# Optimization experiments

Hardware: AMD Instinct MI355X
Metric: run time of the kernel (lower is better)

## Reference

```python
import jax, jax.numpy as jnp
import numpy as np

M, B, S, D, H = 3, 32, 256, 768, 1024
LN_EPS = 1e-5


def _ln(x, g, b):
    m = jnp.mean(x, axis=-1, keepdims=True)
    v = jnp.mean((x - m) ** 2, axis=-1, keepdims=True)
    return (x - m) / jnp.sqrt(v + LN_EPS) * g + b


def setup_inputs() -> dict:
    key = jax.random.key(0)
    ks = jax.random.split(key, 16)
    sc = 0.02  # weight init scale
    return {
        "feats": jax.random.normal(ks[0], (M, B, S, D), jnp.float32),
        "Wq": jax.random.normal(ks[1], (M, D, D), jnp.float32) * sc,
        "bq": jnp.zeros((M, D), jnp.float32),
        "Wk": jax.random.normal(ks[2], (M, D, D), jnp.float32) * sc,
        "bk": jnp.zeros((M, D), jnp.float32),
        "Wv": jax.random.normal(ks[3], (M, D, D), jnp.float32) * sc,
        "bv": jnp.zeros((M, D), jnp.float32),
        "pgq_w": jax.random.normal(ks[4], (M, D), jnp.float32) * sc,
        "pgq_b": jnp.zeros((M,), jnp.float32),
        "pgk_w": jax.random.normal(ks[5], (M, D), jnp.float32) * sc,
        "pgk_b": jnp.zeros((M,), jnp.float32),
        "mu_w": jax.random.normal(ks[6], (M, D), jnp.float32) * sc,
        "mu_b": jnp.zeros((M,), jnp.float32),
        "lv_w": jax.random.normal(ks[7], (M, D), jnp.float32) * sc,
        "lv_b": jnp.zeros((M,), jnp.float32),
        "dyn": jnp.ones((1,), jnp.float32),
        "WE_w": jax.random.normal(ks[8], (M, D, D), jnp.float32) * sc,
        "WE_b": jnp.zeros((M, D), jnp.float32),
        "Wh_w": jax.random.normal(ks[9], (M, D, D), jnp.float32) * sc,
        "Wh_b": jnp.zeros((M, D), jnp.float32),
        "Wqc_w": jax.random.normal(ks[10], (M, D, D), jnp.float32) * sc,
        "Wqc_b": jnp.zeros((M, D), jnp.float32),
        "lnE_g": jnp.ones((M, D), jnp.float32),
        "lnE_b": jnp.zeros((M, D), jnp.float32),
        "lnG_g": jnp.ones((M, D), jnp.float32),
        "lnG_b": jnp.zeros((M, D), jnp.float32),
        "out_w": jax.random.normal(ks[11], (D * M, H), jnp.float32) * sc,
        "out_b": jnp.zeros((H,), jnp.float32),
        "eps": jax.random.normal(ks[12], (M, M - 1, B, S, 1), jnp.float32),
    }


def reference(feats, Wq, bq, Wk, bk, Wv, bv, pgq_w, pgq_b, pgk_w, pgk_b,
              mu_w, mu_b, lv_w, lv_b, dyn, WE_w, WE_b, Wh_w, Wh_b, Wqc_w, Wqc_b,
              lnE_g, lnE_b, lnG_g, lnG_b, out_w, out_b, eps):
    # batched per-modality projections: [M,B,S,D]
    Qs = jnp.einsum('mbsd,mde->mbse', feats, Wq) + bq[:, None, None, :]
    Ks = jnp.einsum('mbsd,mde->mbse', feats, Wk) + bk[:, None, None, :]
    Vs = jnp.einsum('mbsd,mde->mbse', feats, Wv) + bv[:, None, None, :]
    scale = 1.0 / jnp.sqrt(jnp.float32(D))

    kl = jnp.float32(0.0)
    outs = []
    for i in range(M):
        Qi = Qs[i]  # [B,S,D]
        mu = jnp.einsum('bsd,d->bs', Qi, mu_w[i])[..., None] + mu_b[i]      # [B,S,1]
        lv = jnp.einsum('bsd,d->bs', Qi, lv_w[i])[..., None] + lv_b[i]      # [B,S,1]
        std = jnp.exp(0.5 * lv)
        pq_base = jax.nn.sigmoid(
            jnp.einsum('bsd,d->bs', Qi, pgq_w[i])[..., None] + pgq_b[i])    # [B,S,1]
        kl_i = -0.5 * jnp.sum(1.0 + lv - mu ** 2 - jnp.exp(lv))
        agg = jnp.zeros_like(Qi)
        cnt = 0
        for j in range(M):
            if j == i:
                continue
            d_gate = mu + dyn * std * eps[i, cnt]  # reparameterization
            cnt += 1
            kl = kl + kl_i
            g = jax.nn.sigmoid(d_gate)             # [B,S,1]
            p_q = pq_base * g
            p_k = jax.nn.sigmoid(
                jnp.einsum('bsd,d->bs', Ks[j], pgk_w[i])[..., None] + pgk_b[i]) * g
            A = jnp.einsum('bqd,bkd->bqk', Qi, Ks[j]) * scale
            A = A * p_q * jnp.swapaxes(p_k, 1, 2)  # pregated scores
            W = jax.nn.softmax(A, axis=-1)
            agg = agg + jnp.einsum('bqk,bkd->bqd', W, Vs[j])
        # CAG
        E = jax.nn.relu(agg @ WE_w[i] + WE_b[i])
        G = jax.nn.relu(agg @ Wh_w[i] + Wh_b[i] + Qi @ Wqc_w[i] + Wqc_b[i])
        Ci = _ln(E, lnE_g[i], lnE_b[i]) * _ln(G, lnG_g[i], lnG_b[i])
        outs.append(Ci)
    fused = jnp.concatenate(outs, axis=-1)[:, 0, :]  # [B, M*D]
    out = fused @ out_w + out_b                       # [B, H]
    return out, kl
```

## Files before the change

### kernel.cpp

```cpp
#include <hip/hip_runtime.h>

#define M 3
#define B 32
#define S 256
#define D 768
#define H 1024
#define MD (M * D)
#define NP (M * (M - 1))
#define SCALE 0.03608439182435161f
#define LN_EPS 1e-5f

#define OFF_WMU   0
#define OFF_WLV   2304
#define OFF_WPGQ  4608
#define OFF_WPK   6912
#define OFF_CMU   11520
#define OFF_CLV   11523
#define OFF_CPGQ  11526
#define OFF_CPK   11529
#define OFF_MU    11552
#define OFF_LV    36128
#define OFF_PKPRE 60704
#define OFF_PQPRE 109856
#define OFF_Q     109952
#define OFF_QBK   183680
#define OFF_QK    183872
#define OFF_MLH   331328
#define OFF_AGG   332864
#define OFF_E     406592
#define OFF_G     480320
#define OFF_FUSED 554048
#define OFF_KL    627776
#define OFF_FSUM  627840
#define OFF_WKT   1217664
#define OFF_ARENA 2987136
#define OFF_ARENA2 6526080
#define OFF_KLP   11834496

__device__ __forceinline__ float wave_reduce(float v) {
    #pragma unroll
    for (int o = 32; o > 0; o >>= 1) v += __shfl_down(v, o, 64);
    return v;
}

__device__ __forceinline__ float sigmoidf(float x) {
    return 1.0f / (1.0f + __expf(-x));
}

__device__ __forceinline__ float dot4(float4 a, float4 b) {
    return a.x * b.x + a.y * b.y + a.z * b.z + a.w * b.w;
}

__device__ __forceinline__ void fma4(float4& a, float s, float4 w) {
    a.x += s * w.x; a.y += s * w.y; a.z += s * w.z; a.w += s * w.w;
}

__global__ __launch_bounds__(256) void k_prep2(const float* feats,
        const float* Wq, const float* Wk,
        const float* bq, const float* bk,
        const float* mu_w, const float* mu_b, const float* lv_w, const float* lv_b,
        const float* pgq_w, const float* pgq_b, const float* pgk_w, const float* pgk_b,
        float* ws) {
    int blk = blockIdx.x;
    if (blk < 72) {
        int mat = blk / 12, rg = blk % 12;
        const float* Wm; const float *va, *vb, *vc;
        float *oa, *ob, *oc; int nv;
        if (mat < 3) {
            int i = mat;
            Wm = Wq + i * D * D;
            va = mu_w + i * D; vb = lv_w + i * D; vc = pgq_w + i * D;
            oa = ws + OFF_WMU + i * D; ob = ws + OFF_WLV + i * D; oc = ws + OFF_WPGQ + i * D;
            nv = 3;
        } else {
            int j = mat - 3;
            int i1 = (j == 0) ? 1 : 0, i2 = (j == 2) ? 1 : 2;
            int p1 = 2 * i1 + ((j < i1) ? j : j - 1);
            int p2 = 2 * i2 + ((j < i2) ? j : j - 1);
            Wm = Wk + j * D * D;
            va = pgk_w + i1 * D; vb = pgk_w + i2 * D; vc = va;
            oa = ws + OFF_WPK + p1 * D; ob = ws + OFF_WPK + p2 * D; oc = oa;
            nv = 2;
        }
        int wave = threadIdx.x >> 6, lane = threadIdx.x & 63;
        const float4* va4 = (const float4*)va;
        const float4* vb4 = (const float4*)vb;
        const float4* vc4 = (const float4*)vc;
        float4 A0 = va4[lane], A1 = va4[lane + 64], A2 = va4[lane + 128];
        float4 B0 = vb4[lane], B1 = vb4[lane + 64], B2 = vb4[lane + 128];
        float4 C0 = vc4[lane], C1 = vc4[lane + 64], C2 = vc4[lane + 128];
        int base = rg * 64 + wave * 16;
        for (int r = 0; r < 16; r += 2) {
            const float4* rowP = (const float4*)(Wm + (base + r) * D);
            const float4* rowQ = (const float4*)(Wm + (base + r + 1) * D);
            float4 x0 = rowP[lane], x1 = rowP[lane + 64], x2 = rowP[lane + 128];
            float4 y0 = rowQ[lane], y1 = rowQ[lane + 64], y2 = rowQ[lane + 128];
            float daP = dot4(x0, A0) + dot4(x1, A1) + dot4(x2, A2);
            float dbP = dot4(x0, B0) + dot4(x1, B1) + dot4(x2, B2);
            float dcP = dot4(x0, C0) + dot4(x1, C1) + dot4(x2, C2);
            float daQ = dot4(y0, A0) + dot4(y1, A1) + dot4(y2, A2);
            float dbQ = dot4(y0, B0) + dot4(y1, B1) + dot4(y2, B2);
            float dcQ = dot4(y0, C0) + dot4(y1, C1) + dot4(y2, C2);
            daP = wave_reduce(daP); dbP = wave_reduce(dbP);
            daQ = wave_reduce(daQ); dbQ = wave_reduce(dbQ);
            if (nv == 3) { dcP = wave_reduce(dcP); dcQ = wave_reduce(dcQ); }
            if (lane == 0) {
                oa[base + r] = daP; ob[base + r] = dbP;
                oa[base + r + 1] = daQ; ob[base + r + 1] = dbQ;
                if (nv == 3) { oc[base + r] = dcP; oc[base + r + 1] = dcQ; }
            }
        }
    } else if (blk < 87) {
        int job = blk - 72;
        const float *a, *bvec; float bias; float* out;
        if (job < 3)      { int i = job;     a = bq + i * D; bvec = mu_w + i * D;  bias = mu_b[i];  out = ws + OFF_CMU + i; }
        else if (job < 6) { int i = job - 3; a = bq + i * D; bvec = lv_w + i * D;  bias = lv_b[i];  out = ws + OFF_CLV + i; }
        else if (job < 9) { int i = job - 6; a = bq + i * D; bvec = pgq_w + i * D; bias = pgq_b[i]; out = ws + OFF_CPGQ + i; }
        else {
            int p = job - 9, i = p / 2, c = p % 2, j = c + (c >= i ? 1 : 0);
            a = bk + j * D; bvec = pgk_w + i * D; bias = pgk_b[i]; out = ws + OFF_CPK + p;
        }
        int t = threadIdx.x;
        float part = 0.f;
        if (t < 192) part = dot4(((const float4*)a)[t], ((const float4*)bvec)[t]);
        part = wave_reduce(part);
        __shared__ float r[4];
        if ((t & 63) == 0) r[t >> 6] = part;
        __syncthreads();
        if (t == 0) *out = r[0] + r[1] + r[2] + r[3] + bias;
    } else if (blk < 519) {
        int r = blk - 87;
        int j = r / 144; r = r % 144;
        int d0 = (r / 12) * 64, e0 = (r % 12) * 64;
        __shared__ float tile[64][65];
        const float* src = Wk + j * D * D;
        for (int idx = threadIdx.x; idx < 4096; idx += 256) {
            int rr = idx / 64, cc = idx % 64;
            tile[rr][cc] = src[(d0 + rr) * D + e0 + cc];
        }
        __syncthreads();
        float* dst = ws + OFF_WKT + j * D * D;
        for (int idx = threadIdx.x; idx < 4096; idx += 256) {
            int rr = idx / 64, cc = idx % 64;
            dst[(e0 + rr) * D + d0 + cc] = tile[cc][rr];
        }
    } else {
        int qb = blk - 519;
        int i = qb / 96, r = qb % 96, bg = r / 24, kc = r % 24;
        int kbase = kc * 32;
        __shared__ __align__(16) float xs[32][8];
        for (int idx = threadIdx.x; idx < 256; idx += 256) {
            int d = idx & 31, bb = idx >> 5;
            xs[d][bb] = feats[((size_t)(i * B + bg * 8 + bb) * S) * D + kbase + d];
        }
        __syncthreads();
        if (threadIdx.x < 192) {
            int e4 = threadIdx.x * 4;
            const float* Wm = Wq + i * D * D + kbase * D + e4;
            float4 acc[8];
            #pragma unroll
            for (int bb = 0; bb < 8; bb++) acc[bb] = make_float4(0.f, 0.f, 0.f, 0.f);
            for (int k = 0; k < 32; k++) {
                float4 w = *(const float4*)(Wm + k * D);
                float4 x0 = *(const float4*)&xs[k][0];
                float4 x1 = *(const float4*)&xs[k][4];
                fma4(acc[0], x0.x, w); fma4(acc[1], x0.y, w);
                fma4(acc[2], x0.z, w); fma4(acc[3], x0.w, w);
                fma4(acc[4], x1.x, w); fma4(acc[5], x1.y, w);
                fma4(acc[6], x1.z, w); fma4(acc[7], x1.w, w);
            }
            #pragma unroll
            for (int bb = 0; bb < 8; bb++)
                *(float4*)&ws[OFF_ARENA + kc * 73728 + (i * 32 + bg * 8 + bb) * 768 + e4] = acc[bb];
        }
    }
}

__global__ __launch_bounds__(256) void k_redQ(const float* bq, const float* bk, float* ws) {
    int blk = blockIdx.x;
    int i = blk / B, b = blk % B;
    int fbase = (i * B + b) * D;
    int t = threadIdx.x;
    __shared__ float4 qsh[192];
    __shared__ float redsh[8];
    if (t < 192) {
        float4 a = *(const float4*)&bq[i * D + t * 4];
        #pragma unroll
        for (int kc = 0; kc < 24; kc++) {
            float4 v = *(const float4*)&ws[OFF_ARENA + kc * 73728 + fbase + t * 4];
            a.x += v.x; a.y += v.y; a.z += v.z; a.w += v.w;
        }
        *(float4*)&ws[OFF_Q + fbase + t * 4] = a;
        qsh[t] = a;
    }
    __syncthreads();
    int jA = (i == 0) ? 1 : 0, jB = (i == 2) ? 1 : 2;
    float pA_ = 0.f, pB_ = 0.f;
    if (t < 192) {
        float4 q = qsh[t];
        pA_ = dot4(q, *(const float4*)&bk[jA * D + t * 4]);
        pB_ = dot4(q, *(const float4*)&bk[jB * D + t * 4]);
    }
    pA_ = wave_reduce(pA_); pB_ = wave_reduce(pB_);
    int wave = t >> 6, lane = t & 63;
    if (lane == 0) { redsh[wave] = pA_; redsh[4 + wave] = pB_; }
    __syncthreads();
    if (t == 0) {
        ws[OFF_QBK + (2 * i) * B + b]     = redsh[0] + redsh[1] + redsh[2] + redsh[3];
        ws[OFF_QBK + (2 * i + 1) * B + b] = redsh[4] + redsh[5] + redsh[6] + redsh[7];
    }
}

__global__ __launch_bounds__(256) void k_stats2(const float* feats,
        const float* bq, const float* bk, float* ws) {
    int blk = blockIdx.x;
    if (blk < 576) {
        int j = blk / 192, r = blk % 192, vg = r / 24, kc = r % 24;
        int kbase = kc * 32;
        int i1 = (j == 0) ? 1 : 0, i2 = (j == 2) ? 1 : 2;
        __shared__ __align__(16) float xs[32][8];
        for (int idx = threadIdx.x; idx < 256; idx += 256) {
            int d = idx & 31, v = idx >> 5;
            int v64 = vg * 8 + v;
            int i_ = (v64 < 32) ? i1 : i2, b = v64 & 31;
            xs[d][v] = ws[OFF_Q + (i_ * 32 + b) * 768 + kbase + d];
        }
        __syncthreads();
        if (threadIdx.x < 192) {
            int e4 = threadIdx.x * 4;
            const float* Wm = ws + OFF_WKT + j * D * D + kbase * D + e4;
            float4 acc[8];
            #pragma unroll
            for (int bb = 0; bb < 8; bb++) acc[bb] = make_float4(0.f, 0.f, 0.f, 0.f);
            for (int k = 0; k < 32; k++) {
                float4 w = *(const float4*)(Wm + k * D);
                float4 x0 = *(const float4*)&xs[k][0];
                float4 x1 = *(const float4*)&xs[k][4];
                fma4(acc[0], x0.x, w); fma4(acc[1], x0.y, w);
                fma4(acc[2], x0.z, w); fma4(acc[3], x0.w, w);
                fma4(acc[4], x1.x, w); fma4(acc[5], x1.y, w);
                fma4(acc[6], x1.z, w); fma4(acc[7], x1.w, w);
            }
            #pragma unroll
            for (int v = 0; v < 8; v++)
                *(float4*)&ws[OFF_ARENA2 + kc * 147456 + (j * 64 + vg * 8 + v) * 768 + e4] = acc[v];
        }
    } else {
        int blk2 = blk - 576;
        __shared__ float klred[4];
        int wave = threadIdx.x >> 6, lane = threadIdx.x & 63;
        int m = blk2 / 512;
        int row0 = blk2 * 16 + wave * 4;
        int i1 = (m == 0) ? 1 : 0, i2 = (m == 2) ? 1 : 2;
        int p0 = 2 * i1 + ((m < i1) ? m : m - 1);
        int p1 = 2 * i2 + ((m < i2) ? m : m - 1);
        const float4* wmu  = (const float4*)(ws + OFF_WMU + m * D);
        const float4* wlv  = (const float4*)(ws + OFF_WLV + m * D);
        const float4* wpgq = (const float4*)(ws + OFF_WPGQ + m * D);
        const float4* wpk0 = (const float4*)(ws + OFF_WPK + p0 * D);
        const float4* wpk1 = (const float4*)(ws + OFF_WPK + p1 * D);
        float4 U0 = wmu[lane],  U1 = wmu[lane + 64],  U2 = wmu[lane + 128];
        float4 L0 = wlv[lane],  L1 = wlv[lane + 64],  L2 = wlv[lane + 128];
        float4 Q0 = wpgq[lane], Q1 = wpgq[lane + 64], Q2 = wpgq[lane + 128];
        float4 P0 = wpk0[lane], P1 = wpk0[lane + 64], P2 = wpk0[lane + 128];
        float4 R0 = wpk1[lane], R1 = wpk1[lane + 64], R2 = wpk1[lane + 128];
        float4 x[4][3];
        #pragma unroll
        for (int rr = 0; rr < 4; rr++) {
            const float4* f = (const float4*)(feats + (size_t)(row0 + rr) * D);
            x[rr][0] = f[lane]; x[rr][1] = f[lane + 64]; x[rr][2] = f[lane + 128];
        }
        float amu[4], alv[4], apgq[4], apk0[4], apk1[4];
        #pragma unroll
        for (int rr = 0; rr < 4; rr++) {
            amu[rr]  = dot4(x[rr][0], U0) + dot4(x[rr][1], U1) + dot4(x[rr][2], U2);
            alv[rr]  = dot4(x[rr][0], L0) + dot4(x[rr][1], L1) + dot4(x[rr][2], L2);
            apgq[rr] = dot4(x[rr][0], Q0) + dot4(x[rr][1], Q1) + dot4(x[rr][2], Q2);
            apk0[rr] = dot4(x[rr][0], P0) + dot4(x[rr][1], P1) + dot4(x[rr][2], P2);
            apk1[rr] = dot4(x[rr][0], R0) + dot4(x[rr][1], R1) + dot4(x[rr][2], R2);
        }
        #pragma unroll
        for (int rr = 0; rr < 4; rr++) {
            amu[rr] = wave_reduce(amu[rr]);  alv[rr] = wave_reduce(alv[rr]);
            apgq[rr] = wave_reduce(apgq[rr]);
            apk0[rr] = wave_reduce(apk0[rr]); apk1[rr] = wave_reduce(apk1[rr]);
        }
        if (lane == 0) {
            float cmu = ws[OFF_CMU + m], clv = ws[OFF_CLV + m];
            float cpgq = ws[OFF_CPGQ + m];
            float cpk0 = ws[OFF_CPK + p0], cpk1 = ws[OFF_CPK + p1];
            float klsum = 0.f;
            #pragma unroll
            for (int rr = 0; rr < 4; rr++) {
                int row = row0 + rr;
                int rem = row % (B * S);
                int b = rem / S, s = rem % S;
                float muv = amu[rr] + cmu;
                float lvv = alv[rr] + clv;
                ws[OFF_MU + row] = muv;
                ws[OFF_LV + row] = lvv;
                ws[OFF_PKPRE + (p0 * B + b) * S + s] = apk0[rr] + cpk0;
                ws[OFF_PKPRE + (p1 * B + b) * S + s] = apk1[rr] + cpk1;
                if (s == 0) ws[OFF_PQPRE + m * B + b] = apgq[rr] + cpgq;
                klsum += 1.0f + lvv - muv * muv - __expf(lvv);
            }
            klred[wave] = klsum;
        }
        __syncthreads();
        if (threadIdx.x == 0)
            ws[OFF_KLP + blk2] = klred[0] + klred[1] + klred[2] + klred[3];
    }
}

__global__ __launch_bounds__(256) void k_redqk(float* ws) {
    int idx = blockIdx.x * 256 + threadIdx.x;
    int fidx = idx * 4;
    int row = fidx / 768, d = fidx % 768;
    int j = row / 64, v64 = row % 64;
    int b = v64 & 31, islot = v64 >> 5;
    int i_ = islot ? ((j == 2) ? 1 : 2) : ((j == 0) ? 1 : 0);
    int p = 2 * i_ + ((j < i_) ? j : j - 1);
    float4 a = make_float4(0.f, 0.f, 0.f, 0.f);
    #pragma unroll
    for (int kc = 0; kc < 24; kc++) {
        float4 v = *(const float4*)&ws[OFF_ARENA2 + kc * 147456 + fidx];
        a.x += v.x; a.y += v.y; a.z += v.z; a.w += v.w;
    }
    *(float4*)&ws[OFF_QK + (p * B + b) * D + d] = a;
}

__global__ __launch_bounds__(1024) void k_attn(const float* feats, const float* eps,
                                               const float* dyn, float* ws) {
    int blk = blockIdx.x;
    int j = blk / 128, r = blk % 128, b = r >> 2, h = r & 3;
    int i1 = (j == 0) ? 1 : 0, i2 = (j == 2) ? 1 : 2;
    int pA = 2 * i1 + ((j < i1) ? j : j - 1);
    int pB = 2 * i2 + ((j < i2) ? j : j - 1);
    __shared__ __align__(16) float q[2][768];
    __shared__ float pk[2][64];
    __shared__ float sch[2][32], wch[2][32];
    __shared__ float scal[2], pqs[2];
    int t = threadIdx.x;
    float dynv = dyn[0];
    if (t < 384) {
        int slot = t / 192;
        int d4 = (t % 192) * 4;
        int p = slot ? pB : pA;
        *(float4*)&q[slot][d4] = *(const float4*)&ws[OFF_QK + (p * B + b) * D + d4];
    } else if (t < 512) {
        int t2 = t - 384, slot = t2 >> 6, tt = t2 & 63;
        int k = h * 64 + tt;
        int iq = slot ? i2 : i1, p = slot ? pB : pA;
        float mu = ws[OFF_MU + (iq * B + b) * S + k];
        float lv = ws[OFF_LV + (iq * B + b) * S + k];
        float e  = eps[(p * B + b) * S + k];
        float g  = sigmoidf(mu + dynv * __expf(0.5f * lv) * e);
        pk[slot][tt] = sigmoidf(ws[OFF_PKPRE + (p * B + b) * S + k]) * g;
    } else if (t < 514) {
        int slot = t - 512;
        int iq = slot ? i2 : i1, p = slot ? pB : pA;
        float mu0 = ws[OFF_MU + (iq * B + b) * S];
        float lv0 = ws[OFF_LV + (iq * B + b) * S];
        float e0  = eps[(p * B + b) * S];
        float g0  = sigmoidf(mu0 + dynv * __expf(0.5f * lv0) * e0);
        pqs[slot] = sigmoidf(ws[OFF_PQPRE + iq * B + b]) * g0;
    }
    __syncthreads();
    float qbkA = ws[OFF_QBK + pA * B + b];
    float qbkB = ws[OFF_QBK + pB * B + b];
    const float* fb = feats + (size_t)((j * B + b) * S + h * 64) * D;
    float accA = 0.f, accB = 0.f;
    float mloc = -1e30f, lloc = 0.f;
    int w = t >> 6, lane = t & 63;
    for (int c = 0; c < 2; c++) {
        #pragma unroll
        for (int e = 0; e < 2; e++) {
            int rloc = c * 32 + (w << 1) + e;
            const float4* f4 = (const float4*)(fb + (size_t)rloc * D);
            float4 x0 = f4[lane], x1 = f4[lane + 64], x2 = f4[lane + 128];
            const float4* qa4 = (const float4*)&q[0][0];
            const float4* qb4 = (const float4*)&q[1][0];
            float dA = dot4(x0, qa4[lane]) + dot4(x1, qa4[lane + 64]) + dot4(x2, qa4[lane + 128]);
            float dB = dot4(x0, qb4[lane]) + dot4(x1, qb4[lane + 64]) + dot4(x2, qb4[lane + 128]);
            dA = wave_reduce(dA); dB = wave_reduce(dB);
            if (lane == 0) {
                int kk = (w << 1) + e;
                sch[0][kk] = (dA + qbkA) * SCALE * pqs[0] * pk[0][rloc];
                sch[1][kk] = (dB + qbkB) * SCALE * pqs[1] * pk[1][rloc];
            }
        }
        __syncthreads();
        if (t < 64) {
            int slot = t >> 5, kk = t & 31;
            float s = sch[slot][kk];
            float mc = s;
            #pragma unroll
            for (int o = 16; o > 0; o >>= 1) mc = fmaxf(mc, __shfl_xor(mc, o, 64));
            float mn = fmaxf(mloc, mc);
            float f = __expf(mloc - mn);
            float wv = __expf(s - mn);
            float ssum = wv;
            #pragma unroll
            for (int o = 16; o > 0; o >>= 1) ssum += __shfl_xor(ssum, o, 64);
            wch[slot][kk] = wv;
            lloc = lloc * f + ssum;
            mloc = mn;
            if (kk == 0) scal[slot] = f;
        }
        __syncthreads();
        if (t < 768) {
            accA *= scal[0]; accB *= scal[1];
            const float* fcol = fb + (size_t)(c * 32) * D + t;
            #pragma unroll 8
            for (int k = 0; k < 32; k++) {
                float fv = fcol[(size_t)k * D];
                accA += wch[0][k] * fv;
                accB += wch[1][k] * fv;
            }
        }
        __syncthreads();
    }
    if (t < 768) {
        ws[OFF_FSUM + h * 147456 + (pA * B + b) * D + t] = accA;
        ws[OFF_FSUM + h * 147456 + (pB * B + b) * D + t] = accB;
    }
    if (t < 64 && (t & 31) == 0) {
        int slot = t >> 5;
        int p = slot ? pB : pA;
        float* mh = ws + OFF_MLH + (p * B + b) * 8 + h * 2;
        mh[0] = mloc; mh[1] = lloc;
    }
}

__global__ __launch_bounds__(192) void k_agg2(const float* Wv, float* ws) {
    int blk = blockIdx.x;
    int i = blk / 192, r = blk % 192, js = r / 96, r2 = r % 96, bg = r2 / 24, kc = r2 % 24;
    int kbase = kc * 32;
    int j0 = (i == 0) ? 1 : 0, j1 = (i == 2) ? 1 : 2;
    int jv = js ? j1 : j0;
    int p = 2 * i + js;
    __shared__ __align__(16) float xs[32][8];
    __shared__ float comb[4][8];
    if (threadIdx.x < 8) {
        int bb = threadIdx.x;
        const float* mh = ws + OFF_MLH + (p * B + bg * 8 + bb) * 8;
        float m0 = mh[0], l0 = mh[1], m1 = mh[2], l1 = mh[3];
        float m2 = mh[4], l2 = mh[5], m3 = mh[6], l3 = mh[7];
        float Mx = fmaxf(fmaxf(m0, m1), fmaxf(m2, m3));
        float e0 = __expf(m0 - Mx), e1 = __expf(m1 - Mx);
        float e2 = __expf(m2 - Mx), e3 = __expf(m3 - Mx);
        float L = e0 * l0 + e1 * l1 + e2 * l2 + e3 * l3;
        comb[0][bb] = e0 / L; comb[1][bb] = e1 / L;
        comb[2][bb] = e2 / L; comb[3][bb] = e3 / L;
    }
    __syncthreads();
    for (int idx = threadIdx.x; idx < 256; idx += 192) {
        int d = idx & 31, bb = idx >> 5;
        int base = OFF_FSUM + (p * B + bg * 8 + bb) * D + kbase + d;
        xs[d][bb] = comb[0][bb] * ws[base]
                  + comb[1][bb] * ws[base + 147456]
                  + comb[2][bb] * ws[base + 2 * 147456]
                  + comb[3][bb] * ws[base + 3 * 147456];
    }
    __syncthreads();
    int e4 = threadIdx.x * 4;
    const float* W0 = Wv + jv * D * D + kbase * D + e4;
    float4 acc[8];
    #pragma unroll
    for (int bb = 0; bb < 8; bb++) acc[bb] = make_float4(0.f, 0.f, 0.f, 0.f);
    for (int k = 0; k < 32; k++) {
        float4 w0 = *(const float4*)(W0 + k * D);
        float4 a0 = *(const float4*)&xs[k][0];
        float4 a1 = *(const float4*)&xs[k][4];
        fma4(acc[0], a0.x, w0); fma4(acc[1], a0.y, w0);
        fma4(acc[2], a0.z, w0); fma4(acc[3], a0.w, w0);
        fma4(acc[4], a1.x, w0); fma4(acc[5], a1.y, w0);
        fma4(acc[6], a1.z, w0); fma4(acc[7], a1.w, w0);
    }
    #pragma unroll
    for (int bb = 0; bb < 8; bb++)
        *(float4*)&ws[OFF_ARENA + (js * 24 + kc) * 73728 + (i * 32 + bg * 8 + bb) * 768 + e4] = acc[bb];
}

__global__ __launch_bounds__(256) void k_redA(const float* bv, float* ws) {
    int idx = blockIdx.x * 256 + threadIdx.x;
    int fidx = idx * 4;
    int i = fidx / 24576, e = fidx % 768;
    int j0 = (i == 0) ? 1 : 0, j1 = (i == 2) ? 1 : 2;
    float4 b0 = *(const float4*)&bv[j0 * 768 + e];
    float4 b1 = *(const float4*)&bv[j1 * 768 + e];
    float4 a = make_float4(b0.x + b1.x, b0.y + b1.y, b0.z + b1.z, b0.w + b1.w);
    #pragma unroll
    for (int s = 0; s < 48; s++) {
        float4 p = *(const float4*)&ws[OFF_ARENA + s * 73728 + fidx];
        a.x += p.x; a.y += p.y; a.z += p.z; a.w += p.w;
    }
    *(float4*)&ws[OFF_AGG + fidx] = a;
}

__global__ __launch_bounds__(192) void k_eg2(const float* WE_w, const float* Wh_w,
                                             const float* Wqc_w, float* ws) {
    int blk = blockIdx.x;
    int kind = blk / 288, r = blk % 288;
    int i = r / 96, r2 = r % 96, bg = r2 / 24, kc = r2 % 24;
    int kbase = kc * 32;
    int src = (kind == 2) ? OFF_Q : OFF_AGG;
    __shared__ __align__(16) float xs[32][8];
    for (int idx = threadIdx.x; idx < 256; idx += 192) {
        int d = idx & 31, bb = idx >> 5;
        xs[d][bb] = ws[src + (i * 32 + bg * 8 + bb) * 768 + kbase + d];
    }
    __syncthreads();
    int e4 = threadIdx.x * 4;
    const float* Wm = ((kind == 0) ? WE_w : (kind == 1) ? Wh_w : Wqc_w) + i * D * D + kbase * D + e4;
    float4 acc[8];
    #pragma unroll
    for (int bb = 0; bb < 8; bb++) acc[bb] = make_float4(0.f, 0.f, 0.f, 0.f);
    for (int k = 0; k < 32; k++) {
        float4 w = *(const float4*)(Wm + k * D);
        float4 a0 = *(const float4*)&xs[k][0];
        float4 a1 = *(const float4*)&xs[k][4];
        fma4(acc[0], a0.x, w); fma4(acc[1], a0.y, w);
        fma4(acc[2], a0.z, w); fma4(acc[3], a0.w, w);
        fma4(acc[4], a1.x, w); fma4(acc[5], a1.y, w);
        fma4(acc[6], a1.z, w); fma4(acc[7], a1.w, w);
    }
    #pragma unroll
    for (int bb = 0; bb < 8; bb++)
        *(float4*)&ws[OFF_ARENA2 + (kind * 24 + kc) * 73728 + (i * 32 + bg * 8 + bb) * 768 + e4] = acc[bb];
}

__global__ __launch_bounds__(256) void k_redEG(const float* WE_b, const float* Wh_b,
                                               const float* Wqc_b, float* ws) {
    int idx = blockIdx.x * 256 + threadIdx.x;
    int fidx = idx * 4;
    int kind = fidx / 73728;
    int rr = fidx % 73728;
    int i = rr / 24576, e = rr % 768;
    float4 a;
    if (kind == 0) {
        a = *(const float4*)&WE_b[i * 768 + e];
        #pragma unroll
        for (int s = 0; s < 24; s++) {
            float4 p = *(const float4*)&ws[OFF_ARENA2 + s * 73728 + rr];
            a.x += p.x; a.y += p.y; a.z += p.z; a.w += p.w;
        }
    } else {
        float4 b0 = *(const float4*)&Wh_b[i * 768 + e];
        float4 b1 = *(const float4*)&Wqc_b[i * 768 + e];
        a = make_float4(b0.x + b1.x, b0.y + b1.y, b0.z + b1.z, b0.w + b1.w);
        #pragma unroll
        for (int s = 24; s < 72; s++) {
            float4 p = *(const float4*)&ws[OFF_ARENA2 + s * 73728 + rr];
            a.x += p.x; a.y += p.y; a.z += p.z; a.w += p.w;
        }
    }
    a.x = fmaxf(a.x, 0.f); a.y = fmaxf(a.y, 0.f); a.z = fmaxf(a.z, 0.f); a.w = fmaxf(a.w, 0.f);
    *(float4*)&ws[(kind ? OFF_G : OFF_E) + rr] = a;
}

__global__ __launch_bounds__(256) void k_ln2(const float* lnE_g, const float* lnE_b,
        const float* lnG_g, const float* lnG_b, float* ws) {
    int blk = blockIdx.x;
    int i = blk / B, b = blk % B;
    const float* E = ws + OFF_E + (i * B + b) * D;
    const float* G = ws + OFF_G + (i * B + b) * D;
    int t = threadIdx.x;
    float e0 = E[t], e1 = E[t + 256], e2 = E[t + 512];
    float g0 = G[t], g1 = G[t + 256], g2 = G[t + 512];
    __shared__ float r1[256], r2[256], r3[256], r4[256];
    r1[t] = e0 + e1 + e2;
    r2[t] = e0 * e0 + e1 * e1 + e2 * e2;
    r3[t] = g0 + g1 + g2;
    r4[t] = g0 * g0 + g1 * g1 + g2 * g2;
    __syncthreads();
    for (int st = 128; st > 0; st >>= 1) {
        if (t < st) { r1[t] += r1[t + st]; r2[t] += r2[t + st]; r3[t] += r3[t + st]; r4[t] += r4[t + st]; }
        __syncthreads();
    }
    float mE = r1[0] * (1.0f / D), vE = r2[0] * (1.0f / D) - mE * mE;
    float mG = r3[0] * (1.0f / D), vG = r4[0] * (1.0f / D) - mG * mG;
    float sE = rsqrtf(vE + LN_EPS), sG = rsqrtf(vG + LN_EPS);
    float* o = ws + OFF_FUSED + b * MD + i * D;
    const float* eg = lnE_g + i * D; const float* ebv = lnE_b + i * D;
    const float* gg = lnG_g + i * D; const float* gbv = lnG_b + i * D;
    o[t]       = ((e0 - mE) * sE * eg[t]       + ebv[t])       * ((g0 - mG) * sG * gg[t]       + gbv[t]);
    o[t + 256] = ((e1 - mE) * sE * eg[t + 256] + ebv[t + 256]) * ((g1 - mG) * sG * gg[t + 256] + gbv[t + 256]);
    o[t + 512] = ((e2 - mE) * sE * eg[t + 512] + ebv[t + 512]) * ((g2 - mG) * sG * gg[t + 512] + gbv[t + 512]);
}

__global__ __launch_bounds__(256) void k_out2(const float* out_w, float* ws) {
    int blk = blockIdx.x;
    int bg = blk / 72, kc = blk % 72;
    int kbase = kc * 32;
    __shared__ __align__(16) float xs[32][8];
    for (int idx = threadIdx.x; idx < 256; idx += 256) {
        int d = idx & 31, bb = idx >> 5;
        xs[d][bb] = ws[OFF_FUSED + (bg * 8 + bb) * MD + kbase + d];
    }
    __syncthreads();
    int e4 = threadIdx.x * 4;
    const float* Wm = out_w + kbase * H + e4;
    float4 acc[8];
    #pragma unroll
    for (int bb = 0; bb < 8; bb++) acc[bb] = make_float4(0.f, 0.f, 0.f, 0.f);
    for (int k = 0; k < 32; k++) {
        float4 w = *(const float4*)(Wm + k * H);
        float4 x0 = *(const float4*)&xs[k][0];
        float4 x1 = *(const float4*)&xs[k][4];
        fma4(acc[0], x0.x, w); fma4(acc[1], x0.y, w);
        fma4(acc[2], x0.z, w); fma4(acc[3], x0.w, w);
        fma4(acc[4], x1.x, w); fma4(acc[5], x1.y, w);
        fma4(acc[6], x1.z, w); fma4(acc[7], x1.w, w);
    }
    #pragma unroll
    for (int bb = 0; bb < 8; bb++)
        *(float4*)&ws[OFF_ARENA + kc * 32768 + (bg * 8 + bb) * 1024 + e4] = acc[bb];
}

__global__ __launch_bounds__(256) void k_fin(const float* out_b, float* ws, float* out) {
    int b = blockIdx.x;
    int h4 = threadIdx.x * 4;
    float4 a = *(const float4*)&out_b[h4];
    #pragma unroll
    for (int kc = 0; kc < 72; kc++) {
        float4 p = *(const float4*)&ws[OFF_ARENA + kc * 32768 + b * 1024 + h4];
        a.x += p.x; a.y += p.y; a.z += p.z; a.w += p.w;
    }
    *(float4*)&out[b * H + h4] = a;
    if (b == 0) {
        int t = threadIdx.x;
        __shared__ float kls[256];
        float s = 0.f;
        #pragma unroll
        for (int u = 0; u < 6; u++) s += ws[OFF_KLP + t + u * 256];
        kls[t] = s;
        __syncthreads();
        for (int st = 128; st > 0; st >>= 1) {
            if (t < st) kls[t] += kls[t + st];
            __syncthreads();
        }
        if (t == 0) out[B * H] = -kls[0];
    }
}

extern "C" void kernel_launch(void* const* d_in, const int* in_sizes, int n_in,
                              void* d_out, int out_size, void* d_ws, size_t ws_size,
                              hipStream_t stream) {
    const float* feats = (const float*)d_in[0];
    const float* Wq    = (const float*)d_in[1];
    const float* bq    = (const float*)d_in[2];
    const float* Wk    = (const float*)d_in[3];
    const float* bk    = (const float*)d_in[4];
    const float* Wv    = (const float*)d_in[5];
    const float* bv    = (const float*)d_in[6];
    const float* pgq_w = (const float*)d_in[7];
    const float* pgq_b = (const float*)d_in[8];
    const float* pgk_w = (const float*)d_in[9];
    const float* pgk_b = (const float*)d_in[10];
    const float* mu_w  = (const float*)d_in[11];
    const float* mu_b  = (const float*)d_in[12];
    const float* lv_w  = (const float*)d_in[13];
    const float* lv_b  = (const float*)d_in[14];
    const float* dyn   = (const float*)d_in[15];
    const float* WE_w  = (const float*)d_in[16];
    const float* WE_b  = (const float*)d_in[17];
    const float* Wh_w  = (const float*)d_in[18];
    const float* Wh_b  = (const float*)d_in[19];
    const float* Wqc_w = (const float*)d_in[20];
    const float* Wqc_b = (const float*)d_in[21];
    const float* lnE_g = (const float*)d_in[22];
    const float* lnE_b = (const float*)d_in[23];
    const float* lnG_g = (const float*)d_in[24];
    const float* lnG_b = (const float*)d_in[25];
    const float* out_w = (const float*)d_in[26];
    const float* out_b = (const float*)d_in[27];
    const float* eps   = (const float*)d_in[28];
    float* ws  = (float*)d_ws;
    float* out = (float*)d_out;

    k_prep2<<<807, 256, 0, stream>>>(feats, Wq, Wk, bq, bk, mu_w, mu_b, lv_w, lv_b,
                                     pgq_w, pgq_b, pgk_w, pgk_b, ws);
    k_redQ<<<96, 256, 0, stream>>>(bq, bk, ws);
    k_stats2<<<2112, 256, 0, stream>>>(feats, bq, bk, ws);
    k_redqk<<<144, 256, 0, stream>>>(ws);
    k_attn<<<384, 1024, 0, stream>>>(feats, eps, dyn, ws);
    k_agg2<<<576, 192, 0, stream>>>(Wv, ws);
    k_redA<<<72, 256, 0, stream>>>(bv, ws);
    k_eg2<<<864, 192, 0, stream>>>(WE_w, Wh_w, Wqc_w, ws);
    k_redEG<<<144, 256, 0, stream>>>(WE_b, Wh_b, Wqc_b, ws);
    k_ln2<<<96, 256, 0, stream>>>(lnE_g, lnE_b, lnG_g, lnG_b, ws);
    k_out2<<<288, 256, 0, stream>>>(out_w, ws);
    k_fin<<<32, 256, 0, stream>>>(out_b, ws, out);
}
```

Measured before the change: 299.6 us.

## Fuse per-row gate statistics into attention kernel and split keys into eight chunks

```diff
diff --git a/kernel.cpp b/kernel.cpp
--- a/kernel.cpp
+++ b/kernel.cpp
@@ -18,24 +18,20 @@
 #define OFF_CLV   11523
 #define OFF_CPGQ  11526
 #define OFF_CPK   11529
-#define OFF_MU    11552
-#define OFF_LV    36128
-#define OFF_PKPRE 60704
-#define OFF_PQPRE 109856
-#define OFF_Q     109952
-#define OFF_QBK   183680
-#define OFF_QK    183872
-#define OFF_MLH   331328
-#define OFF_AGG   332864
-#define OFF_E     406592
-#define OFF_G     480320
-#define OFF_FUSED 554048
-#define OFF_KL    627776
-#define OFF_FSUM  627840
-#define OFF_WKT   1217664
-#define OFF_ARENA 2987136
-#define OFF_ARENA2 6526080
-#define OFF_KLP   11834496
+#define OFF_PQ    11536
+#define OFF_Q     11776
+#define OFF_QBK   85504
+#define OFF_QK    85760
+#define OFF_MLH   233216
+#define OFF_KLP   236288
+#define OFF_AGG   236544
+#define OFF_E     310272
+#define OFF_G     384000
+#define OFF_FUSED 457728
+#define OFF_FSUM  531520
+#define OFF_WKT   1711168
+#define OFF_ARENA 3480640
+#define OFF_ARENA2 7019584
 
 __device__ __forceinline__ float wave_reduce(float v) {
     #pragma unroll
@@ -176,13 +172,16 @@
     }
 }
 
-__global__ __launch_bounds__(256) void k_redQ(const float* bq, const float* bk, float* ws) {
+__global__ __launch_bounds__(256) void k_redQ(const float* feats, const float* bq,
+        const float* bk, const float* eps, const float* dyn, float* ws) {
     int blk = blockIdx.x;
     int i = blk / B, b = blk % B;
     int fbase = (i * B + b) * D;
     int t = threadIdx.x;
+    int wave = t >> 6, lane = t & 63;
     __shared__ float4 qsh[192];
     __shared__ float redsh[8];
+    __shared__ float pqred[12];
     if (t < 192) {
         float4 a = *(const float4*)&bq[i * D + t * 4];
         #pragma unroll
@@ -202,113 +201,65 @@
         pB_ = dot4(q, *(const float4*)&bk[jB * D + t * 4]);
     }
     pA_ = wave_reduce(pA_); pB_ = wave_reduce(pB_);
-    int wave = t >> 6, lane = t & 63;
     if (lane == 0) { redsh[wave] = pA_; redsh[4 + wave] = pB_; }
+    float dm = 0.f, dl = 0.f, dp = 0.f;
+    if (t < 192) {
+        float4 x = *(const float4*)&feats[((size_t)(i * B + b) * S) * D + t * 4];
+        dm = dot4(x, *(const float4*)&ws[OFF_WMU + i * D + t * 4]);
+        dl = dot4(x, *(const float4*)&ws[OFF_WLV + i * D + t * 4]);
+        dp = dot4(x, *(const float4*)&ws[OFF_WPGQ + i * D + t * 4]);
+    }
+    dm = wave_reduce(dm); dl = wave_reduce(dl); dp = wave_reduce(dp);
+    if (lane == 0 && wave < 3) { pqred[wave] = dm; pqred[4 + wave] = dl; pqred[8 + wave] = dp; }
     __syncthreads();
     if (t == 0) {
         ws[OFF_QBK + (2 * i) * B + b]     = redsh[0] + redsh[1] + redsh[2] + redsh[3];
         ws[OFF_QBK + (2 * i + 1) * B + b] = redsh[4] + redsh[5] + redsh[6] + redsh[7];
-    }
-}
-
-__global__ __launch_bounds__(256) void k_stats2(const float* feats,
-        const float* bq, const float* bk, float* ws) {
-    int blk = blockIdx.x;
-    if (blk < 576) {
-        int j = blk / 192, r = blk % 192, vg = r / 24, kc = r % 24;
-        int kbase = kc * 32;
-        int i1 = (j == 0) ? 1 : 0, i2 = (j == 2) ? 1 : 2;
-        __shared__ __align__(16) float xs[32][8];
-        for (int idx = threadIdx.x; idx < 256; idx += 256) {
-            int d = idx & 31, v = idx >> 5;
-            int v64 = vg * 8 + v;
-            int i_ = (v64 < 32) ? i1 : i2, b = v64 & 31;
-            xs[d][v] = ws[OFF_Q + (i_ * 32 + b) * 768 + kbase + d];
-        }
-        __syncthreads();
-        if (threadIdx.x < 192) {
-            int e4 = threadIdx.x * 4;
-            const float* Wm = ws + OFF_WKT + j * D * D + kbase * D + e4;
-            float4 acc[8];
-            #pragma unroll
-            for (int bb = 0; bb < 8; bb++) acc[bb] = make_float4(0.f, 0.f, 0.f, 0.f);
-            for (int k = 0; k < 32; k++) {
-                float4 w = *(const float4*)(Wm + k * D);
-                float4 x0 = *(const float4*)&xs[k][0];
-                float4 x1 = *(const float4*)&xs[k][4];
-                fma4(acc[0], x0.x, w); fma4(acc[1], x0.y, w);
-                fma4(acc[2], x0.z, w); fma4(acc[3], x0.w, w);
-                fma4(acc[4], x1.x, w); fma4(acc[5], x1.y, w);
-                fma4(acc[6], x1.z, w); fma4(acc[7], x1.w, w);
-            }
-            #pragma unroll
-            for (int v = 0; v < 8; v++)
-                *(float4*)&ws[OFF_ARENA2 + kc * 147456 + (j * 64 + vg * 8 + v) * 768 + e4] = acc[v];
-        }
-    } else {
-        int blk2 = blk - 576;
-        __shared__ float klred[4];
-        int wave = threadIdx.x >> 6, lane = threadIdx.x & 63;
-        int m = blk2 / 512;
-        int row0 = blk2 * 16 + wave * 4;
-        int i1 = (m == 0) ? 1 : 0, i2 = (m == 2) ? 1 : 2;
-        int p0 = 2 * i1 + ((m < i1) ? m : m - 1);
-        int p1 = 2 * i2 + ((m < i2) ? m : m - 1);
-        const float4* wmu  = (const float4*)(ws + OFF_WMU + m * D);
-        const float4* wlv  = (const float4*)(ws + OFF_WLV + m * D);
-        const float4* wpgq = (const float4*)(ws + OFF_WPGQ + m * D);
-        const float4* wpk0 = (const float4*)(ws + OFF_WPK + p0 * D);
-        const float4* wpk1 = (const float4*)(ws + OFF_WPK + p1 * D);
-        float4 U0 = wmu[lane],  U1 = wmu[lane + 64],  U2 = wmu[lane + 128];
-        float4 L0 = wlv[lane],  L1 = wlv[lane + 64],  L2 = wlv[lane + 128];
-        float4 Q0 = wpgq[lane], Q1 = wpgq[lane + 64], Q2 = wpgq[lane + 128];
-        float4 P0 = wpk0[lane], P1 = wpk0[lane + 64], P2 = wpk0[lane + 128];
-        float4 R0 = wpk1[lane], R1 = wpk1[lane + 64], R2 = wpk1[lane + 128];
-        float4 x[4][3];
-        #pragma unroll
-        for (int rr = 0; rr < 4; rr++) {
-            const float4* f = (const float4*)(feats + (size_t)(row0 + rr) * D);
-            x[rr][0] = f[lane]; x[rr][1] = f[lane + 64]; x[rr][2] = f[lane + 128];
-        }
-        float amu[4], alv[4], apgq[4], apk0[4], apk1[4];
-        #pragma unroll
-        for (int rr = 0; rr < 4; rr++) {
-            amu[rr]  = dot4(x[rr][0], U0) + dot4(x[rr][1], U1) + dot4(x[rr][2], U2);
-            alv[rr]  = dot4(x[rr][0], L0) + dot4(x[rr][1], L1) + dot4(x[rr][2], L2);
-            apgq[rr] = dot4(x[rr][0], Q0) + dot4(x[rr][1], Q1) + dot4(x[rr][2], Q2);
-            apk0[rr] = dot4(x[rr][0], P0) + dot4(x[rr][1], P1) + dot4(x[rr][2], P2);
-            apk1[rr] = dot4(x[rr][0], R0) + dot4(x[rr][1], R1) + dot4(x[rr][2], R2);
-        }
-        #pragma unroll
-        for (int rr = 0; rr < 4; rr++) {
-            amu[rr] = wave_reduce(amu[rr]);  alv[rr] = wave_reduce(alv[rr]);
-            apgq[rr] = wave_reduce(apgq[rr]);
-            apk0[rr] = wave_reduce(apk0[rr]); apk1[rr] = wave_reduce(apk1[rr]);
-        }
-        if (lane == 0) {
-            float cmu = ws[OFF_CMU + m], clv = ws[OFF_CLV + m];
-            float cpgq = ws[OFF_CPGQ + m];
-            float cpk0 = ws[OFF_CPK + p0], cpk1 = ws[OFF_CPK + p1];
-            float klsum = 0.f;
-            #pragma unroll
-            for (int rr = 0; rr < 4; rr++) {
-                int row = row0 + rr;
-                int rem = row % (B * S);
-                int b = rem / S, s = rem % S;
-                float muv = amu[rr] + cmu;
-                float lvv = alv[rr] + clv;
-                ws[OFF_MU + row] = muv;
-                ws[OFF_LV + row] = lvv;
-                ws[OFF_PKPRE + (p0 * B + b) * S + s] = apk0[rr] + cpk0;
-                ws[OFF_PKPRE + (p1 * B + b) * S + s] = apk1[rr] + cpk1;
-                if (s == 0) ws[OFF_PQPRE + m * B + b] = apgq[rr] + cpgq;
-                klsum += 1.0f + lvv - muv * muv - __expf(lvv);
-            }
-            klred[wave] = klsum;
-        }
-        __syncthreads();
-        if (threadIdx.x == 0)
-            ws[OFF_KLP + blk2] = klred[0] + klred[1] + klred[2] + klred[3];
+        float mu0 = pqred[0] + pqred[1] + pqred[2] + ws[OFF_CMU + i];
+        float lv0 = pqred[4] + pqred[5] + pqred[6] + ws[OFF_CLV + i];
+        float pqb = pqred[8] + pqred[9] + pqred[10] + ws[OFF_CPGQ + i];
+        float sd = dyn[0] * __expf(0.5f * lv0);
+        float pqs = sigmoidf(pqb);
+        #pragma unroll
+        for (int c = 0; c < 2; c++) {
+            int p = 2 * i + c;
+            float e0 = eps[(size_t)(p * B + b) * S];
+            ws[OFF_PQ + p * B + b] = pqs * sigmoidf(mu0 + sd * e0);
+        }
+    }
+}
+
+__global__ __launch_bounds__(256) void k_qk(float* ws) {
+    int blk = blockIdx.x;
+    int j = blk / 192, r = blk % 192, vg = r / 24, kc = r % 24;
+    int kbase = kc * 32;
+    int i1 = (j == 0) ? 1 : 0, i2 = (j == 2) ? 1 : 2;
+    __shared__ __align__(16) float xs[32][8];
+    for (int idx = threadIdx.x; idx < 256; idx += 256) {
+        int d = idx & 31, v = idx >> 5;
+        int v64 = vg * 8 + v;
+        int i_ = (v64 < 32) ? i1 : i2, b = v64 & 31;
+        xs[d][v] = ws[OFF_Q + (i_ * 32 + b) * 768 + kbase + d];
+    }
+    __syncthreads();
+    if (threadIdx.x < 192) {
+        int e4 = threadIdx.x * 4;
+        const float* Wm = ws + OFF_WKT + j * D * D + kbase * D + e4;
+        float4 acc[8];
+        #pragma unroll
+        for (int bb = 0; bb < 8; bb++) acc[bb] = make_float4(0.f, 0.f, 0.f, 0.f);
+        for (int k = 0; k < 32; k++) {
+            float4 w = *(const float4*)(Wm + k * D);
+            float4 x0 = *(const float4*)&xs[k][0];
+            float4 x1 = *(const float4*)&xs[k][4];
+            fma4(acc[0], x0.x, w); fma4(acc[1], x0.y, w);
+            fma4(acc[2], x0.z, w); fma4(acc[3], x0.w, w);
+            fma4(acc[4], x1.x, w); fma4(acc[5], x1.y, w);
+            fma4(acc[6], x1.z, w); fma4(acc[7], x1.w, w);
+        }
+        #pragma unroll
+        for (int v = 0; v < 8; v++)
+            *(float4*)&ws[OFF_ARENA2 + kc * 147456 + (j * 64 + vg * 8 + v) * 768 + e4] = acc[v];
     }
 }
 
@@ -329,106 +280,113 @@
     *(float4*)&ws[OFF_QK + (p * B + b) * D + d] = a;
 }
 
-__global__ __launch_bounds__(1024) void k_attn(const float* feats, const float* eps,
-                                               const float* dyn, float* ws) {
-    int blk = blockIdx.x;
-    int j = blk / 128, r = blk % 128, b = r >> 2, h = r & 3;
-    int i1 = (j == 0) ? 1 : 0, i2 = (j == 2) ? 1 : 2;
-    int pA = 2 * i1 + ((j < i1) ? j : j - 1);
-    int pB = 2 * i2 + ((j < i2) ? j : j - 1);
-    __shared__ __align__(16) float q[2][768];
-    __shared__ float pk[2][64];
-    __shared__ float sch[2][32], wch[2][32];
-    __shared__ float scal[2], pqs[2];
+__global__ __launch_bounds__(1024) void k_fused(const float* feats, const float* eps,
+                                                const float* dyn, float* ws) {
+    int blk = blockIdx.x;
+    int b = blk >> 3, h = blk & 7;
     int t = threadIdx.x;
+    int w = t >> 6, lane = t & 63;
+    __shared__ __align__(16) float swA[4608];
+    __shared__ __align__(16) float swPK[4608];
+    __shared__ __align__(16) float sqk[4608];
+    __shared__ float raws[6][32], pkps[6][32], mus[3][32], lvs[3][32], wgt[6][32];
+    __shared__ float klv[96];
+    __shared__ float pq_s[6], qbk_s[6], cmu_s[3], clv_s[3], cpk_s[6];
+    {
+        const float4* srcA = (const float4*)(ws + OFF_WMU);
+        const float4* srcP = (const float4*)(ws + OFF_WPK);
+        float4* dA = (float4*)swA;
+        float4* dP = (float4*)swPK;
+        float4* dQ = (float4*)sqk;
+        for (int idx = t; idx < 1152; idx += 1024) {
+            dA[idx] = srcA[idx];
+            dP[idx] = srcP[idx];
+            int p = idx / 192, d4 = (idx % 192) * 4;
+            dQ[idx] = *(const float4*)&ws[OFF_QK + (p * B + b) * D + d4];
+        }
+        if (t < 6) { pq_s[t] = ws[OFF_PQ + t * B + b]; qbk_s[t] = ws[OFF_QBK + t * B + b]; cpk_s[t] = ws[OFF_CPK + t]; }
+        else if (t < 9) { cmu_s[t - 6] = ws[OFF_CMU + t - 6]; clv_s[t - 6] = ws[OFF_CLV + t - 6]; }
+    }
+    __syncthreads();
+    const float4* swA4 = (const float4*)swA;
+    const float4* swPK4 = (const float4*)swPK;
+    const float4* sqk4 = (const float4*)sqk;
+    for (int tau = w * 6; tau < w * 6 + 6; tau++) {
+        int m = tau >> 5, k = tau & 31;
+        const float4* row = (const float4*)(feats + ((size_t)((m * B + b) * S) + h * 32 + k) * D);
+        float4 x0 = row[lane], x1 = row[lane + 64], x2 = row[lane + 128];
+        int i1 = (m == 0) ? 1 : 0, i2 = (m == 2) ? 1 : 2;
+        int pj0 = 2 * i1 + ((m < i1) ? m : m - 1);
+        int pj1 = 2 * i2 + ((m < i2) ? m : m - 1);
+        int oM = m * 192, oL = (3 + m) * 192, o0 = pj0 * 192, o1 = pj1 * 192;
+        float dmu = dot4(x0, swA4[oM + lane]) + dot4(x1, swA4[oM + lane + 64]) + dot4(x2, swA4[oM + lane + 128]);
+        float dlv = dot4(x0, swA4[oL + lane]) + dot4(x1, swA4[oL + lane + 64]) + dot4(x2, swA4[oL + lane + 128]);
+        float dk0 = dot4(x0, swPK4[o0 + lane]) + dot4(x1, swPK4[o0 + lane + 64]) + dot4(x2, swPK4[o0 + lane + 128]);
+        float dk1 = dot4(x0, swPK4[o1 + lane]) + dot4(x1, swPK4[o1 + lane + 64]) + dot4(x2, swPK4[o1 + lane + 128]);
+        float dr0 = dot4(x0, sqk4[o0 + lane]) + dot4(x1, sqk4[o0 + lane + 64]) + dot4(x2, sqk4[o0 + lane + 128]);
+        float dr1 = dot4(x0, sqk4[o1 + lane]) + dot4(x1, sqk4[o1 + lane + 64]) + dot4(x2, sqk4[o1 + lane + 128]);
+        dmu = wave_reduce(dmu); dlv = wave_reduce(dlv);
+        dk0 = wave_reduce(dk0); dk1 = wave_reduce(dk1);
+        dr0 = wave_reduce(dr0); dr1 = wave_reduce(dr1);
+        if (lane == 0) {
+            mus[m][k] = dmu + cmu_s[m];
+            lvs[m][k] = dlv + clv_s[m];
+            pkps[pj0][k] = dk0 + cpk_s[pj0];
+            pkps[pj1][k] = dk1 + cpk_s[pj1];
+            raws[pj0][k] = dr0;
+            raws[pj1][k] = dr1;
+        }
+    }
+    __syncthreads();
     float dynv = dyn[0];
-    if (t < 384) {
-        int slot = t / 192;
-        int d4 = (t % 192) * 4;
-        int p = slot ? pB : pA;
-        *(float4*)&q[slot][d4] = *(const float4*)&ws[OFF_QK + (p * B + b) * D + d4];
-    } else if (t < 512) {
-        int t2 = t - 384, slot = t2 >> 6, tt = t2 & 63;
-        int k = h * 64 + tt;
-        int iq = slot ? i2 : i1, p = slot ? pB : pA;
-        float mu = ws[OFF_MU + (iq * B + b) * S + k];
-        float lv = ws[OFF_LV + (iq * B + b) * S + k];
-        float e  = eps[(p * B + b) * S + k];
-        float g  = sigmoidf(mu + dynv * __expf(0.5f * lv) * e);
-        pk[slot][tt] = sigmoidf(ws[OFF_PKPRE + (p * B + b) * S + k]) * g;
-    } else if (t < 514) {
-        int slot = t - 512;
-        int iq = slot ? i2 : i1, p = slot ? pB : pA;
-        float mu0 = ws[OFF_MU + (iq * B + b) * S];
-        float lv0 = ws[OFF_LV + (iq * B + b) * S];
-        float e0  = eps[(p * B + b) * S];
-        float g0  = sigmoidf(mu0 + dynv * __expf(0.5f * lv0) * e0);
-        pqs[slot] = sigmoidf(ws[OFF_PQPRE + iq * B + b]) * g0;
-    }
-    __syncthreads();
-    float qbkA = ws[OFF_QBK + pA * B + b];
-    float qbkB = ws[OFF_QBK + pB * B + b];
-    const float* fb = feats + (size_t)((j * B + b) * S + h * 64) * D;
-    float accA = 0.f, accB = 0.f;
-    float mloc = -1e30f, lloc = 0.f;
-    int w = t >> 6, lane = t & 63;
-    for (int c = 0; c < 2; c++) {
-        #pragma unroll
-        for (int e = 0; e < 2; e++) {
-            int rloc = c * 32 + (w << 1) + e;
-            const float4* f4 = (const float4*)(fb + (size_t)rloc * D);
-            float4 x0 = f4[lane], x1 = f4[lane + 64], x2 = f4[lane + 128];
-            const float4* qa4 = (const float4*)&q[0][0];
-            const float4* qb4 = (const float4*)&q[1][0];
-            float dA = dot4(x0, qa4[lane]) + dot4(x1, qa4[lane + 64]) + dot4(x2, qa4[lane + 128]);
-            float dB = dot4(x0, qb4[lane]) + dot4(x1, qb4[lane + 64]) + dot4(x2, qb4[lane + 128]);
-            dA = wave_reduce(dA); dB = wave_reduce(dB);
-            if (lane == 0) {
-                int kk = (w << 1) + e;
-                sch[0][kk] = (dA + qbkA) * SCALE * pqs[0] * pk[0][rloc];
-                sch[1][kk] = (dB + qbkB) * SCALE * pqs[1] * pk[1][rloc];
-            }
-        }
-        __syncthreads();
-        if (t < 64) {
-            int slot = t >> 5, kk = t & 31;
-            float s = sch[slot][kk];
-            float mc = s;
-            #pragma unroll
-            for (int o = 16; o > 0; o >>= 1) mc = fmaxf(mc, __shfl_xor(mc, o, 64));
-            float mn = fmaxf(mloc, mc);
-            float f = __expf(mloc - mn);
-            float wv = __expf(s - mn);
-            float ssum = wv;
-            #pragma unroll
-            for (int o = 16; o > 0; o >>= 1) ssum += __shfl_xor(ssum, o, 64);
-            wch[slot][kk] = wv;
-            lloc = lloc * f + ssum;
-            mloc = mn;
-            if (kk == 0) scal[slot] = f;
-        }
-        __syncthreads();
-        if (t < 768) {
-            accA *= scal[0]; accB *= scal[1];
-            const float* fcol = fb + (size_t)(c * 32) * D + t;
+    if (t < 192) {
+        int p = t >> 5, k = t & 31;
+        int iq = p >> 1;
+        float e = eps[(size_t)(p * B + b) * S + h * 32 + k];
+        float g = sigmoidf(mus[iq][k] + dynv * __expf(0.5f * lvs[iq][k]) * e);
+        float pk = sigmoidf(pkps[p][k]) * g;
+        float s = (raws[p][k] + qbk_s[p]) * SCALE * pq_s[p] * pk;
+        float mc = s;
+        #pragma unroll
+        for (int o = 16; o > 0; o >>= 1) mc = fmaxf(mc, __shfl_xor(mc, o, 64));
+        float wv_ = __expf(s - mc);
+        float l = wv_;
+        #pragma unroll
+        for (int o = 16; o > 0; o >>= 1) l += __shfl_xor(l, o, 64);
+        wgt[p][k] = wv_;
+        if (k == 0) {
+            float* mh = ws + OFF_MLH + (p * B + b) * 16 + h * 2;
+            mh[0] = mc; mh[1] = l;
+        }
+    } else if (t < 288) {
+        int tau = t - 192;
+        int m = tau >> 5, k = tau & 31;
+        float muv = mus[m][k], lvv = lvs[m][k];
+        klv[tau] = 1.0f + lvv - muv * muv - __expf(lvv);
+    }
+    __syncthreads();
+    if (t < 768) {
+        #pragma unroll
+        for (int jm = 0; jm < 3; jm++) {
+            int i1 = (jm == 0) ? 1 : 0, i2 = (jm == 2) ? 1 : 2;
+            int pj0 = 2 * i1 + ((jm < i1) ? jm : jm - 1);
+            int pj1 = 2 * i2 + ((jm < i2) ? jm : jm - 1);
+            const float* col = feats + ((size_t)((jm * B + b) * S) + h * 32) * D + t;
+            float accA = 0.f, accB = 0.f;
             #pragma unroll 8
             for (int k = 0; k < 32; k++) {
-                float fv = fcol[(size_t)k * D];
-                accA += wch[0][k] * fv;
-                accB += wch[1][k] * fv;
+                float fv = col[(size_t)k * D];
+                accA += wgt[pj0][k] * fv;
+                accB += wgt[pj1][k] * fv;
             }
-        }
-        __syncthreads();
-    }
-    if (t < 768) {
-        ws[OFF_FSUM + h * 147456 + (pA * B + b) * D + t] = accA;
-        ws[OFF_FSUM + h * 147456 + (pB * B + b) * D + t] = accB;
-    }
-    if (t < 64 && (t & 31) == 0) {
-        int slot = t >> 5;
-        int p = slot ? pB : pA;
-        float* mh = ws + OFF_MLH + (p * B + b) * 8 + h * 2;
-        mh[0] = mloc; mh[1] = lloc;
+            ws[OFF_FSUM + h * 147456 + (pj0 * B + b) * D + t] = accA;
+            ws[OFF_FSUM + h * 147456 + (pj1 * B + b) * D + t] = accB;
+        }
+    }
+    if (t < 64) {
+        float s2 = klv[t] + ((t < 32) ? klv[64 + t] : 0.f);
+        s2 = wave_reduce(s2);
+        if (t == 0) ws[OFF_KLP + blk] = s2;
     }
 }
 
@@ -440,27 +398,29 @@
     int jv = js ? j1 : j0;
     int p = 2 * i + js;
     __shared__ __align__(16) float xs[32][8];
-    __shared__ float comb[4][8];
+    __shared__ float comb[8][8];
     if (threadIdx.x < 8) {
         int bb = threadIdx.x;
-        const float* mh = ws + OFF_MLH + (p * B + bg * 8 + bb) * 8;
-        float m0 = mh[0], l0 = mh[1], m1 = mh[2], l1 = mh[3];
-        float m2 = mh[4], l2 = mh[5], m3 = mh[6], l3 = mh[7];
-        float Mx = fmaxf(fmaxf(m0, m1), fmaxf(m2, m3));
-        float e0 = __expf(m0 - Mx), e1 = __expf(m1 - Mx);
-        float e2 = __expf(m2 - Mx), e3 = __expf(m3 - Mx);
-        float L = e0 * l0 + e1 * l1 + e2 * l2 + e3 * l3;
-        comb[0][bb] = e0 / L; comb[1][bb] = e1 / L;
-        comb[2][bb] = e2 / L; comb[3][bb] = e3 / L;
+        const float* mh = ws + OFF_MLH + (p * B + bg * 8 + bb) * 16;
+        float mm[8], ll[8];
+        float mx = -1e30f;
+        #pragma unroll
+        for (int hh = 0; hh < 8; hh++) { mm[hh] = mh[2 * hh]; ll[hh] = mh[2 * hh + 1]; mx = fmaxf(mx, mm[hh]); }
+        float L = 0.f;
+        float ee[8];
+        #pragma unroll
+        for (int hh = 0; hh < 8; hh++) { ee[hh] = __expf(mm[hh] - mx); L += ee[hh] * ll[hh]; }
+        #pragma unroll
+        for (int hh = 0; hh < 8; hh++) comb[hh][bb] = ee[hh] / L;
     }
     __syncthreads();
     for (int idx = threadIdx.x; idx < 256; idx += 192) {
         int d = idx & 31, bb = idx >> 5;
         int base = OFF_FSUM + (p * B + bg * 8 + bb) * D + kbase + d;
-        xs[d][bb] = comb[0][bb] * ws[base]
-                  + comb[1][bb] * ws[base + 147456]
-                  + comb[2][bb] * ws[base + 2 * 147456]
-                  + comb[3][bb] * ws[base + 3 * 147456];
+        float v = 0.f;
+        #pragma unroll
+        for (int hh = 0; hh < 8; hh++) v += comb[hh][bb] * ws[base + hh * 147456];
+        xs[d][bb] = v;
     }
     __syncthreads();
     int e4 = threadIdx.x * 4;
@@ -631,10 +591,7 @@
     if (b == 0) {
         int t = threadIdx.x;
         __shared__ float kls[256];
-        float s = 0.f;
-        #pragma unroll
-        for (int u = 0; u < 6; u++) s += ws[OFF_KLP + t + u * 256];
-        kls[t] = s;
+        kls[t] = ws[OFF_KLP + t];
         __syncthreads();
         for (int st = 128; st > 0; st >>= 1) {
             if (t < st) kls[t] += kls[t + st];
@@ -681,10 +638,10 @@
 
     k_prep2<<<807, 256, 0, stream>>>(feats, Wq, Wk, bq, bk, mu_w, mu_b, lv_w, lv_b,
                                      pgq_w, pgq_b, pgk_w, pgk_b, ws);
-    k_redQ<<<96, 256, 0, stream>>>(bq, bk, ws);
-    k_stats2<<<2112, 256, 0, stream>>>(feats, bq, bk, ws);
+    k_redQ<<<96, 256, 0, stream>>>(feats, bq, bk, eps, dyn, ws);
+    k_qk<<<576, 256, 0, stream>>>(ws);
     k_redqk<<<144, 256, 0, stream>>>(ws);
-    k_attn<<<384, 1024, 0, stream>>>(feats, eps, dyn, ws);
+    k_fused<<<256, 1024, 0, stream>>>(feats, eps, dyn, ws);
     k_agg2<<<576, 192, 0, stream>>>(Wv, ws);
     k_redA<<<72, 256, 0, stream>>>(bv, ws);
     k_eg2<<<864, 192, 0, stream>>>(WE_w, Wh_w, Wqc_w, ws);
```

Measured after the change: 296.6 us. No clear change (-1.0%).
